# Optimization experiments

Hardware: AMD Instinct MI355X
Metric: run time of the kernel (lower is better)

Reference implementation:

```python
import jax, jax.numpy as jnp
import numpy as np
from jax import lax

VOCAB = 100000
EMB = 300
HID = 512
T = 1024
NUM_LABEL = 20
TAGSET = NUM_LABEL + 2
START = NUM_LABEL
END = NUM_LABEL + 1
NEG = -10000.0


def setup_inputs() -> dict:
    key = jax.random.key(0)
    ks = jax.random.split(key, 16)

    def unif(k, shape, s):
        return jax.random.uniform(k, shape, minval=-s, maxval=s, dtype=jnp.float32)

    inv = 1.0 / np.sqrt(HID)

    def lstm_p(k, in_dim):
        k1, k2, k3, k4 = jax.random.split(k, 4)
        # combined bias b_ih + b_hh (PyTorch has two biases)
        return (unif(k1, (4 * HID, in_dim), inv),
                unif(k2, (4 * HID, HID), inv),
                unif(k3, (4 * HID,), inv) + unif(k4, (4 * HID,), inv))

    enc_f = lstm_p(ks[0], EMB)
    enc_b = lstm_p(ks[1], EMB)
    dec_f = lstm_p(ks[2], 2 * HID)
    dec_b = lstm_p(ks[3], 2 * HID)

    trans = jax.random.normal(ks[4], (TAGSET, TAGSET), dtype=jnp.float32)
    trans = trans.at[START, :].set(NEG).at[:, END].set(NEG)

    lin_s = 1.0 / np.sqrt(2 * HID)
    return {
        "sentence_ids": jax.random.randint(ks[5], (1, T), 0, VOCAB - 1),
        "tags_ids": jax.random.randint(ks[6], (T,), 0, NUM_LABEL),
        "embedding": unif(ks[7], (VOCAB, EMB), 0.1),
        "enc_w_ih_f": enc_f[0], "enc_w_hh_f": enc_f[1], "enc_b_f": enc_f[2],
        "enc_w_ih_b": enc_b[0], "enc_w_hh_b": enc_b[1], "enc_b_b": enc_b[2],
        "dec_w_ih_f": dec_f[0], "dec_w_hh_f": dec_f[1], "dec_b_f": dec_f[2],
        "dec_w_ih_b": dec_b[0], "dec_w_hh_b": dec_b[1], "dec_b_b": dec_b[2],
        "lin_w": unif(ks[8], (TAGSET, 2 * HID), lin_s),
        "lin_b": unif(ks[9], (TAGSET,), lin_s),
        "transitions": trans,
        "h0": jax.random.normal(ks[10], (2, HID), dtype=jnp.float32),
        "c0": jax.random.normal(ks[11], (2, HID), dtype=jnp.float32),
    }


def _lstm(x, w_ih, w_hh, b, h, c, reverse):
    # x: (T, in_dim); PyTorch gate order i, f, g, o
    def step(carry, xt):
        h, c = carry
        g = xt @ w_ih.T + h @ w_hh.T + b  # (4H,)
        i, f, gg, o = jnp.split(g, 4)
        c = jax.nn.sigmoid(f) * c + jax.nn.sigmoid(i) * jnp.tanh(gg)
        h = jax.nn.sigmoid(o) * jnp.tanh(c)
        return (h, c), h
    _, hs = lax.scan(step, (h, c), x, reverse=reverse)
    return hs  # (T, H)


def _bilstm(x, pf, pb, h0, c0):
    hf = _lstm(x, pf[0], pf[1], pf[2], h0[0], c0[0], False)
    hb = _lstm(x, pb[0], pb[1], pb[2], h0[1], c0[1], True)
    return jnp.concatenate([hf, hb], axis=-1)  # (T, 2H)


def reference(sentence_ids, tags_ids, embedding,
              enc_w_ih_f, enc_w_hh_f, enc_b_f, enc_w_ih_b, enc_w_hh_b, enc_b_b,
              dec_w_ih_f, dec_w_hh_f, dec_b_f, dec_w_ih_b, dec_w_hh_b, dec_b_b,
              lin_w, lin_b, transitions, h0, c0):
    x = embedding[sentence_ids[0]]  # (T, EMB), batch=1 hard-coded as in torch code
    enc = _bilstm(x, (enc_w_ih_f, enc_w_hh_f, enc_b_f),
                  (enc_w_ih_b, enc_w_hh_b, enc_b_b), h0, c0)
    dec = _bilstm(enc, (dec_w_ih_f, dec_w_hh_f, dec_b_f),
                  (dec_w_ih_b, dec_w_hh_b, dec_b_b), h0, c0)
    feats = dec @ lin_w.T + lin_b  # (T, TAGSET)

    alpha0 = jnp.full((TAGSET,), NEG, dtype=jnp.float32).at[START].set(0.0)

    # CRF forward algorithm (log-sum-exp recurrence)
    def fstep(alpha, feat):
        return jax.nn.logsumexp(alpha[:, None] + transitions + feat[None, :], axis=0), None
    alpha, _ = lax.scan(fstep, alpha0, feats)
    fwd_score = jax.nn.logsumexp(alpha + transitions[:, END])[None]  # (1,)

    # gold path score
    tags = jnp.concatenate([jnp.array([START], dtype=tags_ids.dtype), tags_ids.reshape(-1)])
    gold = (transitions[tags[:-1], tags[1:]].sum()
            + feats[jnp.arange(feats.shape[0]), tags[1:]].sum()
            + transitions[tags[-1], END])
    loss = fwd_score - gold  # (1,)

    # Viterbi decode
    def vstep(alpha, feat):
        smat = alpha[:, None] + feat[None, :] + transitions
        return jnp.max(smat, axis=0), jnp.argmax(smat, axis=0)
    valpha, bps = lax.scan(vstep, alpha0, feats)
    best_last = jnp.argmax(valpha + transitions[:, END])

    def bstep(tag, bp):
        prev = bp[tag]
        return prev, prev
    _, path_head = lax.scan(bstep, best_last, bps[1:], reverse=True)  # path[0..T-2]
    tag_seq = jnp.concatenate([path_head, best_last[None]]).astype(jnp.int32)  # (T,)

    return (tag_seq, loss)
```

## Files before the change

### kernel.cpp

```cpp
#include <hip/hip_runtime.h>
#include <hip/hip_bf16.h>
#include <math.h>

#define T_LEN   1024
#define EMB     300
#define EMBP    320
#define HID     512
#define TAGSET  22
#define START_TAG 20
#define END_TAG   21
#define NWG     32
#define SENT    0xFFFFFFFFu

typedef float f32x4 __attribute__((ext_vector_type(4)));

__device__ __forceinline__ float sigf(float x) { return 1.f / (1.f + expf(-x)); }

__global__ void gather_pad_x(const int* __restrict__ ids, const float* __restrict__ emb,
                             float* __restrict__ xp) {
    int t = blockIdx.x;
    int id = ids[t];
    for (int k = threadIdx.x; k < EMBP; k += blockDim.x)
        xp[t * EMBP + k] = (k < EMB) ? emb[(size_t)id * EMB + k] : 0.f;
}

__global__ void pad_w(const float* __restrict__ w, float* __restrict__ wp) {
    int r = blockIdx.x;
    for (int k = threadIdx.x; k < EMBP; k += blockDim.x)
        wp[r * EMBP + k] = (k < EMB) ? w[(size_t)r * EMB + k] : 0.f;
}

#define BM 64
#define BN 64
#define BK 32
__launch_bounds__(256)
__global__ void gemm_nt(const float* __restrict__ A, const float* __restrict__ B,
                        const float* __restrict__ bias, float* __restrict__ C,
                        int K, int ldc) {
    __shared__ float As[BK][BM + 4];
    __shared__ float Bs[BK][BN + 4];
    const int bm = blockIdx.y * BM, bn = blockIdx.x * BN;
    const int tid = threadIdx.x;
    const int tx = tid & 15, ty = tid >> 4;
    const int lrow = tid >> 2, lk = (tid & 3) * 8;
    float acc[4][4] = {};
    for (int k0 = 0; k0 < K; k0 += BK) {
        float4 a0 = *(const float4*)(A + (size_t)(bm + lrow) * K + k0 + lk);
        float4 a1 = *(const float4*)(A + (size_t)(bm + lrow) * K + k0 + lk + 4);
        float4 b0 = *(const float4*)(B + (size_t)(bn + lrow) * K + k0 + lk);
        float4 b1 = *(const float4*)(B + (size_t)(bn + lrow) * K + k0 + lk + 4);
        __syncthreads();
        As[lk + 0][lrow] = a0.x; As[lk + 1][lrow] = a0.y;
        As[lk + 2][lrow] = a0.z; As[lk + 3][lrow] = a0.w;
        As[lk + 4][lrow] = a1.x; As[lk + 5][lrow] = a1.y;
        As[lk + 6][lrow] = a1.z; As[lk + 7][lrow] = a1.w;
        Bs[lk + 0][lrow] = b0.x; Bs[lk + 1][lrow] = b0.y;
        Bs[lk + 2][lrow] = b0.z; Bs[lk + 3][lrow] = b0.w;
        Bs[lk + 4][lrow] = b1.x; Bs[lk + 5][lrow] = b1.y;
        Bs[lk + 6][lrow] = b1.z; Bs[lk + 7][lrow] = b1.w;
        __syncthreads();
        #pragma unroll
        for (int kk = 0; kk < BK; ++kk) {
            float4 av = *(const float4*)&As[kk][ty * 4];
            float4 bv = *(const float4*)&Bs[kk][tx * 4];
            acc[0][0] += av.x * bv.x; acc[0][1] += av.x * bv.y; acc[0][2] += av.x * bv.z; acc[0][3] += av.x * bv.w;
            acc[1][0] += av.y * bv.x; acc[1][1] += av.y * bv.y; acc[1][2] += av.y * bv.z; acc[1][3] += av.y * bv.w;
            acc[2][0] += av.z * bv.x; acc[2][1] += av.z * bv.y; acc[2][2] += av.z * bv.z; acc[2][3] += av.z * bv.w;
            acc[3][0] += av.w * bv.x; acc[3][1] += av.w * bv.y; acc[3][2] += av.w * bv.z; acc[3][3] += av.w * bv.w;
        }
    }
    const int n = bn + tx * 4;
    #pragma unroll
    for (int i = 0; i < 4; ++i) {
        float4 o;
        o.x = acc[i][0] + bias[n + 0];
        o.y = acc[i][1] + bias[n + 1];
        o.z = acc[i][2] + bias[n + 2];
        o.w = acc[i][3] + bias[n + 3];
        *(float4*)(C + (size_t)(bm + ty * 4 + i) * ldc + n) = o;
    }
}

#define W_LIST(F) F(0) F(1) F(2) F(3) F(4) F(5) F(6) F(7) \
                  F(8) F(9) F(10) F(11) F(12) F(13) F(14) F(15) \
                  F(16) F(17) F(18) F(19) F(20) F(21) F(22) F(23) \
                  F(24) F(25) F(26) F(27) F(28) F(29) F(30) F(31)
#define DECLW(n) f32x4 W##n = wr4[n];
#define PINW(n)  asm volatile("" : "+v"(W##n));
#define DOTW(n, A) { f32x4 hv = hp4[n]; \
    A += W##n[0]*hv[0] + W##n[1]*hv[1] + W##n[2]*hv[2] + W##n[3]*hv[3]; }

__launch_bounds__(256, 1)
__global__ void lstm_rec(const float* __restrict__ whh_f, const float* __restrict__ whh_b,
                         const float* __restrict__ pre_f, const float* __restrict__ pre_b,
                         const float* __restrict__ h0, const float* __restrict__ c0,
                         float* __restrict__ hout) {
    const int dir = blockIdx.x >> 5;
    const int w   = blockIdx.x & 31;
    const float* whh = dir ? whh_b : whh_f;
    const float* pre = dir ? pre_b : pre_f;
    const int tid = threadIdx.x;
    const int lr = tid >> 2, q = tid & 3;
    const int g = lr >> 4, j = lr & 15;
    const int grow = g * 512 + w * 16 + j;

    const f32x4* wr4 = (const f32x4*)(whh + (size_t)grow * 512 + q * 128);
    W_LIST(DECLW)
    W_LIST(PINW)

    __shared__ float hs[4 * 132];
    __shared__ float gd[4][16];
    float c_reg = 0.f;
    if (tid < 16) c_reg = c0[dir * 512 + w * 16 + tid];
    const int col = dir * 512;

    for (int t = 0; t < 1024; ++t) {
        const int pos = dir ? (1023 - t) : t;
        float pf_i = 0.f, pf_f = 0.f, pf_g = 0.f, pf_o = 0.f;
        if (tid < 16) {
            const float* pr = pre + (size_t)pos * 2048 + w * 16 + tid;
            pf_i = pr[0]; pf_f = pr[512]; pf_g = pr[1024]; pf_o = pr[1536];
        }
        if (tid < 64) {
            unsigned v[8];
            if (t == 0) {
                const float* src = h0 + dir * 512 + tid * 8;
                #pragma unroll
                for (int i = 0; i < 8; ++i) v[i] = __float_as_uint(src[i]);
            } else {
                const unsigned* src =
                    (const unsigned*)(hout + (size_t)(dir ? pos + 1 : pos - 1) * 1024 + col) + tid * 8;
                bool done = false;
                unsigned long long pend;
                do {
                    if (!done) {
                        #pragma unroll
                        for (int i = 0; i < 8; ++i)
                            v[i] = __hip_atomic_load(&src[i], __ATOMIC_RELAXED,
                                                     __HIP_MEMORY_SCOPE_AGENT);
                        done = true;
                        #pragma unroll
                        for (int i = 0; i < 8; ++i) done = done && (v[i] != SENT);
                    }
                    pend = __ballot(!done);
                } while (pend);
            }
            const int qq = tid >> 4, base = (tid & 15) * 8;
            #pragma unroll
            for (int i = 0; i < 8; ++i) hs[qq * 132 + base + i] = __uint_as_float(v[i]);
        }
        __syncthreads();
        const f32x4* hp4 = (const f32x4*)&hs[q * 132];
        float ac0 = 0.f, ac1 = 0.f, ac2 = 0.f, ac3 = 0.f;
        DOTW(0, ac0)  DOTW(1, ac1)  DOTW(2, ac2)  DOTW(3, ac3)
        DOTW(4, ac0)  DOTW(5, ac1)  DOTW(6, ac2)  DOTW(7, ac3)
        DOTW(8, ac0)  DOTW(9, ac1)  DOTW(10, ac2) DOTW(11, ac3)
        DOTW(12, ac0) DOTW(13, ac1) DOTW(14, ac2) DOTW(15, ac3)
        DOTW(16, ac0) DOTW(17, ac1) DOTW(18, ac2) DOTW(19, ac3)
        DOTW(20, ac0) DOTW(21, ac1) DOTW(22, ac2) DOTW(23, ac3)
        DOTW(24, ac0) DOTW(25, ac1) DOTW(26, ac2) DOTW(27, ac3)
        DOTW(28, ac0) DOTW(29, ac1) DOTW(30, ac2) DOTW(31, ac3)
        float acc = (ac0 + ac1) + (ac2 + ac3);
        acc += __shfl_xor(acc, 1);
        acc += __shfl_xor(acc, 2);
        if (q == 0) gd[g][j] = acc;
        __syncthreads();
        if (tid < 16) {
            float gi = gd[0][tid] + pf_i;
            float gf = gd[1][tid] + pf_f;
            float gg = gd[2][tid] + pf_g;
            float go = gd[3][tid] + pf_o;
            float c = sigf(gf) * c_reg + sigf(gi) * tanhf(gg);
            float h = sigf(go) * tanhf(c);
            c_reg = c;
            __hip_atomic_store(&hout[(size_t)pos * 1024 + col + w * 16 + tid], h,
                               __ATOMIC_RELAXED, __HIP_MEMORY_SCOPE_AGENT);
        }
    }
}

__global__ void feats_kernel(const float* __restrict__ dc, const float* __restrict__ lw,
                             const float* __restrict__ lb, float* __restrict__ ft) {
    const int t = blockIdx.x;
    const int tid = threadIdx.x;
    const int j = tid >> 3, s = tid & 7;
    if (j >= TAGSET) return;
    const float4* a = (const float4*)(dc + (size_t)t * 1024);
    const float4* wv = (const float4*)(lw + (size_t)j * 1024);
    float acc = 0.f;
    #pragma unroll
    for (int i = 0; i < 32; ++i) {
        float4 av = a[s + 8 * i];
        float4 ww = wv[s + 8 * i];
        acc += av.x * ww.x + av.y * ww.y + av.z * ww.z + av.w * ww.w;
    }
    acc += __shfl_xor(acc, 1);
    acc += __shfl_xor(acc, 2);
    acc += __shfl_xor(acc, 4);
    if (s == 0) ft[t * TAGSET + j] = acc + lb[j];
}

#define TR_LIST(F) F(0) F(1) F(2) F(3) F(4) F(5) F(6) F(7) F(8) F(9) F(10) \
                   F(11) F(12) F(13) F(14) F(15) F(16) F(17) F(18) F(19) F(20) F(21)
#define DECLTR(i) float trc##i = trans[i * TAGSET + jj];
#define VDEF(i)   float v##i = sm[i] + trc##i;
#define ESUM(i)   e##i = __expf(v##i - m);
#define MAXTREE(m) { \
    float m0 = fmaxf(v0, v1),  m1 = fmaxf(v2, v3),  m2_ = fmaxf(v4, v5),  m3 = fmaxf(v6, v7); \
    float m4 = fmaxf(v8, v9),  m5 = fmaxf(v10, v11), m6 = fmaxf(v12, v13), m7 = fmaxf(v14, v15); \
    float m8 = fmaxf(v16, v17), m9 = fmaxf(v18, v19), m10 = fmaxf(v20, v21); \
    float n0 = fmaxf(m0, m1), n1 = fmaxf(m2_, m3), n2 = fmaxf(m4, m5), n3 = fmaxf(m6, m7); \
    float n4 = fmaxf(m8, m9); \
    float p0 = fmaxf(n0, n1), p1 = fmaxf(n2, n3), p2 = fmaxf(n4, m10); \
    m = fmaxf(fmaxf(p0, p1), p2); }
#define VITSTEP(i) { float v_ = sm[i] + trc##i; \
    if (v_ > best) { best = v_; arg = i; } }

__launch_bounds__(128)
__global__ void crf_kernel(const float* __restrict__ ft, const float* __restrict__ trans,
                           const int* __restrict__ tags, float* __restrict__ out) {
    __shared__ float tr[TAGSET * TAGSET];
    __shared__ unsigned char bps[1024][TAGSET];
    __shared__ float res[2];
    const int tid = threadIdx.x;
    for (int i = tid; i < TAGSET * TAGSET; i += blockDim.x) tr[i] = trans[i];
    __syncthreads();

    if (blockIdx.x == 0) {
        if (tid < 64) {
            __shared__ float sm[32];
            const int j = tid;
            const int jj = (j < TAGSET) ? j : 0;
            TR_LIST(DECLTR)
            float trEnd = trans[jj * TAGSET + END_TAG];
            float alpha = (j == START_TAG) ? 0.f : -10000.f;
            float ftc = ft[jj];
            for (int t = 0; t < 1024; ++t) {
                float ftn = (t < 1023) ? ft[(t + 1) * TAGSET + jj] : 0.f;
                if (j < TAGSET) sm[j] = alpha;
                TR_LIST(VDEF)
                float m; MAXTREE(m)
                float e0,e1,e2,e3,e4,e5,e6,e7,e8,e9,e10,e11,e12,e13,e14,e15,e16,e17,e18,e19,e20,e21;
                TR_LIST(ESUM)
                float s0 = ((e0+e1)+(e2+e3)) + ((e4+e5)+(e6+e7));
                float s1 = ((e8+e9)+(e10+e11)) + ((e12+e13)+(e14+e15));
                float s2 = ((e16+e17)+(e18+e19)) + (e20+e21);
                alpha = ftc + m + __logf((s0 + s1) + s2);
                ftc = ftn;
            }
            float v = (j < TAGSET) ? (alpha + trEnd) : -3.0e38f;
            float m2 = v;
            for (int d = 1; d < 32; d <<= 1) m2 = fmaxf(m2, __shfl_xor(m2, d));
            float e = (j < TAGSET) ? __expf(v - m2) : 0.f;
            for (int d = 1; d < 32; d <<= 1) e += __shfl_xor(e, d);
            if (tid == 0) res[0] = m2 + __logf(e);
        } else {
            const int l = tid - 64;
            float gsum = 0.f;
            for (int t = l; t < 1024; t += 64) {
                int cur = tags[t];
                int prev = (t == 0) ? START_TAG : tags[t - 1];
                gsum += tr[prev * TAGSET + cur] + ft[t * TAGSET + cur];
            }
            for (int d = 1; d < 64; d <<= 1) gsum += __shfl_xor(gsum, d);
            if (l == 0) res[1] = gsum + tr[tags[1023] * TAGSET + END_TAG];
        }
        __syncthreads();
        if (tid == 0) out[1024] = res[0] - res[1];
    } else {
        if (tid < 64) {
            __shared__ float sm[32];
            const int j = tid;
            const int jj = (j < TAGSET) ? j : 0;
            TR_LIST(DECLTR)
            float trEnd = trans[jj * TAGSET + END_TAG];
            float a = (j == START_TAG) ? 0.f : -10000.f;
            float ftc = ft[jj];
            for (int t = 0; t < 1024; ++t) {
                float ftn = (t < 1023) ? ft[(t + 1) * TAGSET + jj] : 0.f;
                if (j < TAGSET) sm[j] = a;
                float best = -3.4e38f; int arg = 0;
                VITSTEP(0)  VITSTEP(1)  VITSTEP(2)  VITSTEP(3)  VITSTEP(4)  VITSTEP(5)
                VITSTEP(6)  VITSTEP(7)  VITSTEP(8)  VITSTEP(9)  VITSTEP(10) VITSTEP(11)
                VITSTEP(12) VITSTEP(13) VITSTEP(14) VITSTEP(15) VITSTEP(16) VITSTEP(17)
                VITSTEP(18) VITSTEP(19) VITSTEP(20) VITSTEP(21)
                if (j < TAGSET) bps[t][j] = (unsigned char)arg;
                a = best + ftc;
                ftc = ftn;
            }
            float v = (j < TAGSET) ? (a + trEnd) : -3.4e38f;
            float bb = -3.4e38f; int bl = 0;
            for (int i = 0; i < TAGSET; ++i) {
                float vi = __shfl(v, i);
                if (vi > bb) { bb = vi; bl = i; }
            }
            __threadfence_block();
            if (tid == 0) {
                int cur = bl;
                out[1023] = (float)cur;
                for (int t = 1023; t >= 1; --t) {
                    cur = bps[t][cur];
                    out[t - 1] = (float)cur;
                }
            }
        }
    }
}

extern "C" void kernel_launch(void* const* d_in, const int* in_sizes, int n_in,
                              void* d_out, int out_size, void* d_ws, size_t ws_size,
                              hipStream_t stream) {
    const int*   ids   = (const int*)d_in[0];
    const int*   tags  = (const int*)d_in[1];
    const float* emb   = (const float*)d_in[2];
    const float* e_wif = (const float*)d_in[3];
    const float* e_whf = (const float*)d_in[4];
    const float* e_bf  = (const float*)d_in[5];
    const float* e_wib = (const float*)d_in[6];
    const float* e_whb = (const float*)d_in[7];
    const float* e_bb  = (const float*)d_in[8];
    const float* d_wif = (const float*)d_in[9];
    const float* d_whf = (const float*)d_in[10];
    const float* d_bf  = (const float*)d_in[11];
    const float* d_wib = (const float*)d_in[12];
    const float* d_whb = (const float*)d_in[13];
    const float* d_bb  = (const float*)d_in[14];
    const float* lw    = (const float*)d_in[15];
    const float* lb    = (const float*)d_in[16];
    const float* trp   = (const float*)d_in[17];
    const float* h0    = (const float*)d_in[18];
    const float* c0    = (const float*)d_in[19];
    float* out = (float*)d_out;

    float* ws    = (float*)d_ws;
    float* xp    = ws;
    float* wpf   = xp    + 1024 * 320;
    float* wpb   = wpf   + 2048 * 320;
    float* pre_f = wpb   + 2048 * 320;
    float* pre_b = pre_f + 1024 * 2048;
    float* ecat  = pre_b + 1024 * 2048;
    float* dcat  = ecat  + 1024 * 1024;
    float* ft    = dcat  + 1024 * 1024;

    hipMemsetAsync(ecat, 0xFF, 1024 * 1024 * sizeof(float), stream);
    hipMemsetAsync(dcat, 0xFF, 1024 * 1024 * sizeof(float), stream);

    gather_pad_x<<<1024, 256, 0, stream>>>(ids, emb, xp);
    pad_w<<<2048, 256, 0, stream>>>(e_wif, wpf);
    pad_w<<<2048, 256, 0, stream>>>(e_wib, wpb);

    dim3 gg(2048 / BN, 1024 / BM);
    gemm_nt<<<gg, 256, 0, stream>>>(xp, wpf, e_bf, pre_f, EMBP, 2048);
    gemm_nt<<<gg, 256, 0, stream>>>(xp, wpb, e_bb, pre_b, EMBP, 2048);

    lstm_rec<<<64, 256, 0, stream>>>(e_whf, e_whb, pre_f, pre_b, h0, c0, ecat);

    gemm_nt<<<gg, 256, 0, stream>>>(ecat, d_wif, d_bf, pre_f, 1024, 2048);
    gemm_nt<<<gg, 256, 0, stream>>>(ecat, d_wib, d_bb, pre_b, 1024, 2048);

    lstm_rec<<<64, 256, 0, stream>>>(d_whf, d_whb, pre_f, pre_b, h0, c0, dcat);

    feats_kernel<<<1024, 256, 0, stream>>>(dcat, lw, lb, ft);
    crf_kernel<<<2, 128, 0, stream>>>(ft, trp, tags, out);
}
```

Baseline: 4.539 ms.

## Split LSTM recurrence over 128 workgroups with wave-local gate reduction

The recurrent LSTM kernel now uses 64 workgroups per direction instead of 32, with each thread holding 16 weight vectors instead of 32. The four gates for a hidden unit are computed and reduced within a single wave using shuffles, which removes the second __syncthreads and the shared gate buffer. The per-step h broadcast uses a double-buffered LDS array plus a workgroup-scope flag that the other waves spin on, replacing a barrier. In exchange, more workgroups poll global memory for the previous h at every step, and spin-waiting inside the workgroup adds its own contention.

New measurement: 6.403 ms. 1.41x slower.

```diff
diff --git a/kernel.cpp b/kernel.cpp
--- a/kernel.cpp
+++ b/kernel.cpp
@@ -9,7 +9,6 @@
 #define TAGSET  22
 #define START_TAG 20
 #define END_TAG   21
-#define NWG     32
 #define SENT    0xFFFFFFFFu
 
 typedef float f32x4 __attribute__((ext_vector_type(4)));
@@ -81,10 +80,8 @@
     }
 }
 
-#define W_LIST(F) F(0) F(1) F(2) F(3) F(4) F(5) F(6) F(7) \
-                  F(8) F(9) F(10) F(11) F(12) F(13) F(14) F(15) \
-                  F(16) F(17) F(18) F(19) F(20) F(21) F(22) F(23) \
-                  F(24) F(25) F(26) F(27) F(28) F(29) F(30) F(31)
+#define W16_LIST(F) F(0) F(1) F(2) F(3) F(4) F(5) F(6) F(7) \
+                    F(8) F(9) F(10) F(11) F(12) F(13) F(14) F(15)
 #define DECLW(n) f32x4 W##n = wr4[n];
 #define PINW(n)  asm volatile("" : "+v"(W##n));
 #define DOTW(n, A) { f32x4 hv = hp4[n]; \
@@ -95,41 +92,51 @@
                          const float* __restrict__ pre_f, const float* __restrict__ pre_b,
                          const float* __restrict__ h0, const float* __restrict__ c0,
                          float* __restrict__ hout) {
-    const int dir = blockIdx.x >> 5;
-    const int w   = blockIdx.x & 31;
+    const int bid = blockIdx.x;
+    const int dir = bid >> 6;
+    const int w   = bid & 63;
     const float* whh = dir ? whh_b : whh_f;
     const float* pre = dir ? pre_b : pre_f;
     const int tid = threadIdx.x;
-    const int lr = tid >> 2, q = tid & 3;
-    const int g = lr >> 4, j = lr & 15;
-    const int grow = g * 512 + w * 16 + j;
-
-    const f32x4* wr4 = (const f32x4*)(whh + (size_t)grow * 512 + q * 128);
-    W_LIST(DECLW)
-    W_LIST(PINW)
-
-    __shared__ float hs[4 * 132];
-    __shared__ float gd[4][16];
+    const int wv  = tid >> 6;
+    const int ln  = tid & 63;
+    const int hh  = ln >> 5;
+    const int g   = (ln >> 3) & 3;
+    const int e   = ln & 7;
+    const int hidx = w * 8 + wv * 2 + hh;
+    const int grow = g * 512 + hidx;
+
+    const f32x4* wr4 = (const f32x4*)(whh + (size_t)grow * 512 + e * 64);
+    W16_LIST(DECLW)
+    W16_LIST(PINW)
+
+    __shared__ float hs[2][544];
+    __shared__ int sflag;
+    if (tid == 0) sflag = 0;
+    __syncthreads();
+
+    const bool isprod = (g == 0 && e == 0);
     float c_reg = 0.f;
-    if (tid < 16) c_reg = c0[dir * 512 + w * 16 + tid];
+    if (isprod) c_reg = c0[dir * 512 + hidx];
     const int col = dir * 512;
 
     for (int t = 0; t < 1024; ++t) {
         const int pos = dir ? (1023 - t) : t;
         float pf_i = 0.f, pf_f = 0.f, pf_g = 0.f, pf_o = 0.f;
-        if (tid < 16) {
-            const float* pr = pre + (size_t)pos * 2048 + w * 16 + tid;
+        if (isprod) {
+            const float* pr = pre + (size_t)pos * 2048 + hidx;
             pf_i = pr[0]; pf_f = pr[512]; pf_g = pr[1024]; pf_o = pr[1536];
         }
-        if (tid < 64) {
+        const int buf = t & 1;
+        if (wv == 0) {
             unsigned v[8];
             if (t == 0) {
-                const float* src = h0 + dir * 512 + tid * 8;
+                const float* src = h0 + dir * 512 + ln * 8;
                 #pragma unroll
                 for (int i = 0; i < 8; ++i) v[i] = __float_as_uint(src[i]);
             } else {
                 const unsigned* src =
-                    (const unsigned*)(hout + (size_t)(dir ? pos + 1 : pos - 1) * 1024 + col) + tid * 8;
+                    (const unsigned*)(hout + (size_t)(dir ? pos + 1 : pos - 1) * 1024 + col) + ln * 8;
                 bool done = false;
                 unsigned long long pend;
                 do {
@@ -145,35 +152,37 @@
                     pend = __ballot(!done);
                 } while (pend);
             }
-            const int qq = tid >> 4, base = (tid & 15) * 8;
+            const int base = (ln >> 3) * 68 + (ln & 7) * 8;
+            f32x4 w0, w1;
             #pragma unroll
-            for (int i = 0; i < 8; ++i) hs[qq * 132 + base + i] = __uint_as_float(v[i]);
-        }
-        __syncthreads();
-        const f32x4* hp4 = (const f32x4*)&hs[q * 132];
+            for (int i = 0; i < 4; ++i) { w0[i] = __uint_as_float(v[i]); w1[i] = __uint_as_float(v[i + 4]); }
+            *(f32x4*)&hs[buf][base] = w0;
+            *(f32x4*)&hs[buf][base + 4] = w1;
+            __hip_atomic_store(&sflag, t + 1, __ATOMIC_RELEASE, __HIP_MEMORY_SCOPE_WORKGROUP);
+        } else {
+            while (__hip_atomic_load(&sflag, __ATOMIC_ACQUIRE, __HIP_MEMORY_SCOPE_WORKGROUP) < t + 1) {}
+        }
+        const f32x4* hp4 = (const f32x4*)&hs[buf][e * 68];
         float ac0 = 0.f, ac1 = 0.f, ac2 = 0.f, ac3 = 0.f;
         DOTW(0, ac0)  DOTW(1, ac1)  DOTW(2, ac2)  DOTW(3, ac3)
         DOTW(4, ac0)  DOTW(5, ac1)  DOTW(6, ac2)  DOTW(7, ac3)
         DOTW(8, ac0)  DOTW(9, ac1)  DOTW(10, ac2) DOTW(11, ac3)
         DOTW(12, ac0) DOTW(13, ac1) DOTW(14, ac2) DOTW(15, ac3)
-        DOTW(16, ac0) DOTW(17, ac1) DOTW(18, ac2) DOTW(19, ac3)
-        DOTW(20, ac0) DOTW(21, ac1) DOTW(22, ac2) DOTW(23, ac3)
-        DOTW(24, ac0) DOTW(25, ac1) DOTW(26, ac2) DOTW(27, ac3)
-        DOTW(28, ac0) DOTW(29, ac1) DOTW(30, ac2) DOTW(31, ac3)
         float acc = (ac0 + ac1) + (ac2 + ac3);
         acc += __shfl_xor(acc, 1);
         acc += __shfl_xor(acc, 2);
-        if (q == 0) gd[g][j] = acc;
-        __syncthreads();
-        if (tid < 16) {
-            float gi = gd[0][tid] + pf_i;
-            float gf = gd[1][tid] + pf_f;
-            float gg = gd[2][tid] + pf_g;
-            float go = gd[3][tid] + pf_o;
+        acc += __shfl_xor(acc, 4);
+        const int gb = ln & 32;
+        float gi = __shfl(acc, gb + 0);
+        float gf = __shfl(acc, gb + 8);
+        float gg = __shfl(acc, gb + 16);
+        float go = __shfl(acc, gb + 24);
+        if (isprod) {
+            gi += pf_i; gf += pf_f; gg += pf_g; go += pf_o;
             float c = sigf(gf) * c_reg + sigf(gi) * tanhf(gg);
             float h = sigf(go) * tanhf(c);
             c_reg = c;
-            __hip_atomic_store(&hout[(size_t)pos * 1024 + col + w * 16 + tid], h,
+            __hip_atomic_store(&hout[(size_t)pos * 1024 + col + hidx], h,
                                __ATOMIC_RELAXED, __HIP_MEMORY_SCOPE_AGENT);
         }
     }
@@ -353,12 +362,12 @@
     gemm_nt<<<gg, 256, 0, stream>>>(xp, wpf, e_bf, pre_f, EMBP, 2048);
     gemm_nt<<<gg, 256, 0, stream>>>(xp, wpb, e_bb, pre_b, EMBP, 2048);
 
-    lstm_rec<<<64, 256, 0, stream>>>(e_whf, e_whb, pre_f, pre_b, h0, c0, ecat);
+    lstm_rec<<<128, 256, 0, stream>>>(e_whf, e_whb, pre_f, pre_b, h0, c0, ecat);
 
     gemm_nt<<<gg, 256, 0, stream>>>(ecat, d_wif, d_bf, pre_f, 1024, 2048);
     gemm_nt<<<gg, 256, 0, stream>>>(ecat, d_wib, d_bb, pre_b, 1024, 2048);
 
-    lstm_rec<<<64, 256, 0, stream>>>(d_whf, d_whb, pre_f, pre_b, h0, c0, dcat);
+    lstm_rec<<<128, 256, 0, stream>>>(d_whf, d_whb, pre_f, pre_b, h0, c0, dcat);
 
     feats_kernel<<<1024, 256, 0, stream>>>(dcat, lw, lb, ft);
     crf_kernel<<<2, 128, 0, stream>>>(ft, trp, tags, out);
```
